# Performance work log

Hardware: AMD Instinct MI355X
Metric: run time of the kernel (lower is better)

The kernel has to match this reference:

```python
import jax, jax.numpy as jnp
import numpy as np
import math

B, S, HID = 2, 2048, 1024
NH = 16
HD = HID // NH


def setup_inputs() -> dict:
    key = jax.random.key(0)
    ks = jax.random.split(key, 5)
    std = 1.0 / math.sqrt(HID)
    return {
        "x": jax.random.normal(ks[0], (B, S, HID), dtype=jnp.float32),
        "wq": jax.random.normal(ks[1], (HID, HID), dtype=jnp.float32) * std,
        "wk": jax.random.normal(ks[2], (HID, HID), dtype=jnp.float32) * std,
        "wv": jax.random.normal(ks[3], (HID, HID), dtype=jnp.float32) * std,
        "wo": jax.random.normal(ks[4], (HID, HID), dtype=jnp.float32) * std,
    }


def reference(x, wq, wk, wv, wo):
    # x: [B, S, HID]; weights stored as nn.Linear weight [out, in] -> y = x @ W.T
    b, s, _ = x.shape
    scale = 1.0 / math.sqrt(HD)

    def heads(t):  # [B, S, HID] -> [B, NH, S, HD]
        return t.reshape(b, s, NH, HD).transpose(0, 2, 1, 3)

    q = heads(x @ wq.T)
    k = heads(x @ wk.T)
    v = heads(x @ wv.T)

    # single ring step (cp_size=1): streaming-LSE causal attention
    scores = jnp.einsum("bhqd,bhkd->bhqk", q, k) * scale  # [B, NH, S, S]
    q_idx = jnp.arange(s)[:, None]
    k_idx = jnp.arange(s)[None, :]
    causal_mask = k_idx > q_idx  # [S, S]
    scores = jnp.where(causal_mask, -jnp.inf, scores)

    local_max = jnp.max(scores, axis=-1, keepdims=True)
    exp_scores = jnp.exp(scores - local_max)
    local_sum = jnp.sum(exp_scores, axis=-1, keepdims=True)
    attn_num = jnp.einsum("bhqk,bhkd->bhqd", exp_scores, v)
    attn_out = attn_num / (local_sum + 1e-8)  # [B, NH, S, HD]

    attn_out = attn_out.transpose(0, 2, 1, 3).reshape(b, s, HID)
    return attn_out @ wo.T
```

## Files before the change

kernel.cpp:

```cpp
#include <hip/hip_runtime.h>
#include <hip/hip_bf16.h>

#define S_LEN 2048
#define NHEAD 16
#define HDIM 64
#define HID 1024
#define BATCH 2
#define TSTR 136

typedef __attribute__((ext_vector_type(8))) short s16x8;
typedef __attribute__((ext_vector_type(4))) short s16x4;
typedef __attribute__((ext_vector_type(4))) float f32x4;

__device__ __forceinline__ short f2bf(float f) {
    union { __hip_bfloat16 b; short s; } u;
    u.b = __float2bfloat16(f);
    return u.s;
}
__device__ __forceinline__ float fexp2(float x) {
    return __builtin_amdgcn_exp2f(x);
}
__device__ __forceinline__ f32x4 mfma16(s16x8 a, s16x8 b, f32x4 c) {
    return __builtin_amdgcn_mfma_f32_16x16x32_bf16(a, b, c, 0, 0, 0);
}
__device__ __forceinline__ void gload16(const short* g, short* l) {
    __builtin_amdgcn_global_load_lds(
        (const __attribute__((address_space(1))) void*)g,
        (__attribute__((address_space(3))) void*)l, 16, 0, 0);
}
__device__ __forceinline__ unsigned bfpack(float a, float b) {
    unsigned ua = __builtin_bit_cast(unsigned, a) + 0x8000u;
    unsigned ub = __builtin_bit_cast(unsigned, b) + 0x8000u;
    return (ub & 0xFFFF0000u) | (ua >> 16);
}

__global__ __launch_bounds__(256) void convert_kernel(
    const float* __restrict__ x,  const float* __restrict__ wq,
    const float* __restrict__ wk, const float* __restrict__ wv,
    const float* __restrict__ wo,
    short* __restrict__ xb, short* __restrict__ wcat, short* __restrict__ wob)
{
    const int F4X = 1048576, F4W = 262144;
    const int total = F4X + 4 * F4W;
    for (int i = blockIdx.x * blockDim.x + threadIdx.x; i < total;
         i += gridDim.x * blockDim.x) {
        const float4* s; short* d; int off;
        if (i < F4X)              { s = (const float4*)x;  d = xb;             off = i; }
        else if (i < F4X + F4W)   { s = (const float4*)wq; d = wcat;           off = i - F4X; }
        else if (i < F4X + 2*F4W) { s = (const float4*)wk; d = wcat + 1048576; off = i - (F4X + F4W); }
        else if (i < F4X + 3*F4W) { s = (const float4*)wv; d = wcat + 2097152; off = i - (F4X + 2*F4W); }
        else                      { s = (const float4*)wo; d = wob;            off = i - (F4X + 3*F4W); }
        float4 v = s[off];
        s16x4 o4 = { f2bf(v.x), f2bf(v.y), f2bf(v.z), f2bf(v.w) };
        *(s16x4*)(d + (size_t)off * 4) = o4;
    }
}

__global__ __launch_bounds__(256) void qkv_gemm2(
    const short* __restrict__ xb, const short* __restrict__ wcat,
    short* __restrict__ q_ws, short* __restrict__ k_ws, short* __restrict__ vt_ws)
{
    __shared__ union SM {
        struct { short A[128][64]; short B[128][64]; } s;
        short T[128][TSTR];
    } sm;
    const int t = threadIdx.x;
    const int lane = t & 63, w = t >> 6;
    const int g = lane >> 4, r15 = lane & 15;
    const int wm = w >> 1, wn = w & 1;
    const int bid = blockIdx.x;
    const int cx = bid & 7, ii = bid >> 3;
    const int mt = cx * 4 + (ii & 3), nt = ii >> 2;
    const int m0 = mt * 128, n0 = nt * 128;
    const int sel = n0 >> 10;
    const int nr0 = n0 & 1023;
    const short* Ag = (sel == 2) ? (wcat + (size_t)(2048 + nr0) * 1024)
                                 : (xb   + (size_t)m0 * 1024);
    const short* Bg = (sel == 2) ? (xb   + (size_t)m0 * 1024)
                                 : (wcat + (size_t)(sel * 1024 + nr0) * 1024);
    const int lrow = lane >> 3;
    const int scol = ((lane & 7) ^ lrow) * 8;
    const int rsw = r15 & 7;
    const float osc = (sel == 0) ? 0.125f : ((sel == 1) ? 1.44269504f : 1.0f);

    f32x4 acc[4][4] = {};

    for (int k0 = 0; k0 < 1024; k0 += 64) {
        __syncthreads();
        #pragma unroll
        for (int ch = 0; ch < 4; ++ch) {
            const int row = w * 32 + ch * 8;
            gload16(Ag + (size_t)(row + lrow) * 1024 + k0 + scol, &sm.s.A[row][0]);
            gload16(Bg + (size_t)(row + lrow) * 1024 + k0 + scol, &sm.s.B[row][0]);
        }
        __syncthreads();
        #pragma unroll
        for (int kk = 0; kk < 2; ++kk) {
            s16x8 af[4], bfr[4];
            #pragma unroll
            for (int mi = 0; mi < 4; ++mi)
                af[mi] = *(const s16x8*)&sm.s.A[wm * 64 + mi * 16 + r15][((kk * 4 + g) ^ rsw) * 8];
            #pragma unroll
            for (int ni = 0; ni < 4; ++ni)
                bfr[ni] = *(const s16x8*)&sm.s.B[wn * 64 + ni * 16 + r15][((kk * 4 + g) ^ rsw) * 8];
            #pragma unroll
            for (int mi = 0; mi < 4; ++mi)
                #pragma unroll
                for (int ni = 0; ni < 4; ++ni)
                    acc[mi][ni] = mfma16(af[mi], bfr[ni], acc[mi][ni]);
        }
    }

    __syncthreads();
    #pragma unroll
    for (int mi = 0; mi < 4; ++mi)
    #pragma unroll
    for (int ni = 0; ni < 4; ++ni)
        #pragma unroll
        for (int reg = 0; reg < 4; ++reg)
            sm.T[wm * 64 + mi * 16 + g * 4 + reg][wn * 64 + ni * 16 + r15]
                = f2bf(acc[mi][ni][reg] * osc);
    __syncthreads();

    const int b = m0 >> 11;
    const int ms = m0 & 2047;
    #pragma unroll
    for (int it = 0; it < 8; ++it) {
        int u = w + it * 4;
        int half = u & 1;
        int rg = u >> 1;
        int r = rg * 8 + lrow;
        int colc = half * 64 + (lane & 7) * 8;
        s16x8 v = *(const s16x8*)&sm.T[r][colc];
        if (sel == 2) {
            int n = nr0 + r;
            int h = n >> 6, d = n & 63;
            *(s16x8*)(vt_ws + ((size_t)(b * NHEAD + h) * HDIM + d) * S_LEN + ms + colc) = v;
        } else {
            int s = ms + r;
            int n = nr0 + colc;
            int h = n >> 6, d = n & 63;
            short* dst = (sel == 0) ? q_ws : k_ws;
            *(s16x8*)(dst + ((size_t)(b * NHEAD + h) * S_LEN + s) * HDIM + d) = v;
        }
    }
}

__global__ __launch_bounds__(256) void attn_kernel11(
    const short* __restrict__ q_ws, const short* __restrict__ k_ws,
    const short* __restrict__ vt_ws, short* __restrict__ attn_ws)
{
    __shared__ short Ks[2][64][64];
    __shared__ short Vts[2][64][64];
    const int t = threadIdx.x;
    const int lane = t & 63, w = t >> 6;
    const int g = lane >> 4, r15 = lane & 15;
    const int bid = blockIdx.x;
    const int lb = (bid & 7) * 32 + (bid >> 3);
    const int pi = lb & 7;
    const int bh = lb >> 3;
    const size_t base = (size_t)bh * S_LEN * HDIM;
    const int swr = (r15 & 7) << 3;
    const int b = bh >> 4, h = bh & 15;

    const int r0 = t >> 3, c0 = (t & 7) * 8;
    const int cx0 = c0 ^ ((r0 & 7) << 3);

    union P8 { unsigned u[4]; s16x8 v; };
    union V8 { s16x4 h[2]; s16x8 v; };

    for (int phase = 0; phase < 2; ++phase) {
        const int qt = phase ? (15 - pi) : pi;
        const int q0 = qt * 128;
        const int ntk = 2 * qt + 2;
        const int dgt = 2 * qt + (w >> 1);
        const int qrel = (w & 1) * 32 + r15;

        s16x8 qf[2][2];
        #pragma unroll
        for (int m = 0; m < 2; ++m)
            #pragma unroll
            for (int c = 0; c < 2; ++c)
                qf[m][c] = *(const s16x8*)(q_ws + base +
                    (size_t)(q0 + w * 32 + m * 16 + r15) * HDIM + c * 32 + g * 8);
        f32x4 o[2][4] = {};
        float lr[2] = { 0.f, 0.f };

        #pragma unroll
        for (int j = 0; j < 2; ++j) {
            int r = r0 + j * 32;
            *(s16x8*)&Ks[0][r][cx0]  = *(const s16x8*)(k_ws  + base + (size_t)r * HDIM + c0);
            *(s16x8*)&Vts[0][r][cx0] = *(const s16x8*)(vt_ws + base + (size_t)r * S_LEN + c0);
        }
        __syncthreads();

        const short* kp = k_ws  + base + (size_t)(64 + r0) * HDIM + c0;
        const short* vp = vt_ws + base + (size_t)r0 * S_LEN + 64 + c0;

        for (int kt = 0; kt < ntk; ++kt) {
            const int cur = kt & 1;
            const bool pre = (kt + 1 < ntk);
            s16x8 ka[2], va[2];
            if (pre) {
                ka[0] = *(const s16x8*)kp;
                ka[1] = *(const s16x8*)(kp + (size_t)32 * HDIM);
                va[0] = *(const s16x8*)vp;
                va[1] = *(const s16x8*)(vp + (size_t)32 * S_LEN);
                kp += (size_t)64 * HDIM; vp += 64;
            }

            if (kt <= dgt) {
                const bool dg = (kt == dgt);

                s16x8 kfa[4][2];
                #pragma unroll
                for (int f = 0; f < 4; ++f)
                    #pragma unroll
                    for (int c = 0; c < 2; ++c)
                        kfa[f][c] = *(const s16x8*)&Ks[cur][f * 16 + r15][(c * 32 + g * 8) ^ swr];
                V8 vfr[4][2];
                #pragma unroll
                for (int f2 = 0; f2 < 4; ++f2)
                    #pragma unroll
                    for (int kc = 0; kc < 2; ++kc) {
                        vfr[f2][kc].h[0] = *(const s16x4*)&Vts[cur][f2 * 16 + r15][(kc * 32 + g * 4) ^ swr];
                        vfr[f2][kc].h[1] = *(const s16x4*)&Vts[cur][f2 * 16 + r15][(kc * 32 + 16 + g * 4) ^ swr];
                    }

                #pragma unroll
                for (int m = 0; m < 2; ++m) {
                    f32x4 z[4];
                    __builtin_amdgcn_s_setprio(1);
                    #pragma unroll
                    for (int f = 0; f < 4; ++f) {
                        f32x4 zz = { 0.f, 0.f, 0.f, 0.f };
                        zz = mfma16(kfa[f][0], qf[m][0], zz);
                        zz = mfma16(kfa[f][1], qf[m][1], zz);
                        z[f] = zz;
                    }
                    __builtin_amdgcn_s_setprio(0);

                    if (dg) {
                        const int qr = qrel + m * 16;
                        #pragma unroll
                        for (int f = 0; f < 4; ++f)
                            #pragma unroll
                            for (int reg = 0; reg < 4; ++reg)
                                if (f * 16 + g * 4 + reg > qr) z[f][reg] = -3e30f;
                    }

                    P8 p8[2];
                    #pragma unroll
                    for (int f = 0; f < 4; ++f) {
                        float e0 = fexp2(z[f][0]);
                        float e1 = fexp2(z[f][1]);
                        float e2 = fexp2(z[f][2]);
                        float e3 = fexp2(z[f][3]);
                        lr[m] += (e0 + e1) + (e2 + e3);
                        p8[f >> 1].u[(f & 1) * 2]     = bfpack(e0, e1);
                        p8[f >> 1].u[(f & 1) * 2 + 1] = bfpack(e2, e3);
                    }

                    __builtin_amdgcn_s_setprio(1);
                    #pragma unroll
                    for (int f2 = 0; f2 < 4; ++f2) {
                        o[m][f2] = mfma16(vfr[f2][0].v, p8[0].v, o[m][f2]);
                        o[m][f2] = mfma16(vfr[f2][1].v, p8[1].v, o[m][f2]);
                    }
                    __builtin_amdgcn_s_setprio(0);
                }
            }

            if (pre) {
                #pragma unroll
                for (int j = 0; j < 2; ++j) {
                    int r = r0 + j * 32;
                    *(s16x8*)&Ks[cur ^ 1][r][cx0]  = ka[j];
                    *(s16x8*)&Vts[cur ^ 1][r][cx0] = va[j];
                }
            }
            __syncthreads();
        }

        #pragma unroll
        for (int m = 0; m < 2; ++m) {
            float l = lr[m];
            l += __shfl_xor(l, 16);
            l += __shfl_xor(l, 32);
            float inv = 1.f / (l + 1e-8f);
            const int qg = q0 + w * 32 + m * 16 + r15;
            size_t obase = ((size_t)b * S_LEN + qg) * HID + h * HDIM + g * 4;
            #pragma unroll
            for (int f2 = 0; f2 < 4; ++f2) {
                s16x4 ov = { f2bf(o[m][f2][0] * inv), f2bf(o[m][f2][1] * inv),
                             f2bf(o[m][f2][2] * inv), f2bf(o[m][f2][3] * inv) };
                *(s16x4*)(attn_ws + obase + f2 * 16) = ov;
            }
        }
        __syncthreads();
    }
}

__global__ __launch_bounds__(256) void wo_gemm2(
    const short* __restrict__ attn, const short* __restrict__ wob,
    float* __restrict__ out)
{
    __shared__ short As[128][64];
    __shared__ short Bs[128][64];
    const int t = threadIdx.x;
    const int lane = t & 63, w = t >> 6;
    const int g = lane >> 4, r15 = lane & 15;
    const int wm = w >> 1, wn = w & 1;
    const int bid = blockIdx.x;
    const int cx = bid & 7, ii = bid >> 3;
    const int mt = cx * 4 + (ii & 3), nt = ii >> 2;
    const int m0 = mt * 128, n0 = nt * 128;
    const int lrow = lane >> 3;
    const int scol = ((lane & 7) ^ lrow) * 8;
    const int rsw = r15 & 7;

    f32x4 acc[4][4] = {};

    for (int k0 = 0; k0 < 1024; k0 += 64) {
        __syncthreads();
        #pragma unroll
        for (int ch = 0; ch < 4; ++ch) {
            const int row = w * 32 + ch * 8;
            gload16(attn + (size_t)(m0 + row + lrow) * 1024 + k0 + scol, &As[row][0]);
            gload16(wob  + (size_t)(n0 + row + lrow) * 1024 + k0 + scol, &Bs[row][0]);
        }
        __syncthreads();
        #pragma unroll
        for (int kk = 0; kk < 2; ++kk) {
            s16x8 af[4], bfr[4];
            #pragma unroll
            for (int mi = 0; mi < 4; ++mi)
                af[mi] = *(const s16x8*)&As[wm * 64 + mi * 16 + r15][((kk * 4 + g) ^ rsw) * 8];
            #pragma unroll
            for (int ni = 0; ni < 4; ++ni)
                bfr[ni] = *(const s16x8*)&Bs[wn * 64 + ni * 16 + r15][((kk * 4 + g) ^ rsw) * 8];
            #pragma unroll
            for (int mi = 0; mi < 4; ++mi)
                #pragma unroll
                for (int ni = 0; ni < 4; ++ni)
                    acc[mi][ni] = mfma16(af[mi], bfr[ni], acc[mi][ni]);
        }
    }

    #pragma unroll
    for (int mi = 0; mi < 4; ++mi)
    #pragma unroll
    for (int ni = 0; ni < 4; ++ni) {
        #pragma unroll
        for (int reg = 0; reg < 4; ++reg) {
            int m = m0 + wm * 64 + mi * 16 + g * 4 + reg;
            int n = n0 + wn * 64 + ni * 16 + r15;
            out[(size_t)m * 1024 + n] = acc[mi][ni][reg];
        }
    }
}

extern "C" void kernel_launch(void* const* d_in, const int* in_sizes, int n_in,
                              void* d_out, int out_size, void* d_ws, size_t ws_size,
                              hipStream_t stream) {
    const float* x  = (const float*)d_in[0];
    const float* wq = (const float*)d_in[1];
    const float* wk = (const float*)d_in[2];
    const float* wv = (const float*)d_in[3];
    const float* wo = (const float*)d_in[4];
    float* out = (float*)d_out;

    const size_t ELEMS = (size_t)BATCH * S_LEN * HID;
    short* q_ws    = (short*)d_ws;
    short* k_ws    = q_ws + ELEMS;
    short* vt_ws   = k_ws + ELEMS;
    short* xb      = vt_ws + ELEMS;
    short* attn_ws = xb;
    short* wcat    = xb + ELEMS;
    short* wob     = wcat + 3145728;

    convert_kernel<<<dim3(2048), dim3(256), 0, stream>>>(x, wq, wk, wv, wo, xb, wcat, wob);
    qkv_gemm2<<<dim3(768), dim3(256), 0, stream>>>(xb, wcat, q_ws, k_ws, vt_ws);
    attn_kernel11<<<dim3(256), dim3(256), 0, stream>>>(q_ws, k_ws, vt_ws, attn_ws);
    wo_gemm2<<<dim3(256), dim3(256), 0, stream>>>(attn_ws, wob, out);
}
```

Measured before the change: 117.5 us.

## Software-pipeline attention by deferring PV MFMAs one key tile

The attention loop now issues the P·V matrix multiplies for the previous key tile at the start of the next iteration, before the QK^T and exp work for the current tile. The loop is unrolled by two, with ping-pong V fragment register buffers, and probabilities are kept in registers for both row groups. A tail step finishes the last deferred PV for the warps whose last active tile is the final one. The aim is to overlap the exp/pack vector work with matrix-core work and hide LDS-read latency, at the cost of more live registers and possibly lower occupancy.

```diff
diff --git a/kernel.cpp b/kernel.cpp
--- a/kernel.cpp
+++ b/kernel.cpp
@@ -33,6 +33,9 @@
     unsigned ub = __builtin_bit_cast(unsigned, b) + 0x8000u;
     return (ub & 0xFFFF0000u) | (ua >> 16);
 }
+
+union P8 { unsigned u[4]; s16x8 v; };
+union V8 { s16x4 h[2]; s16x8 v; };
 
 __global__ __launch_bounds__(256) void convert_kernel(
     const float* __restrict__ x,  const float* __restrict__ wq,
@@ -146,7 +149,7 @@
     }
 }
 
-__global__ __launch_bounds__(256) void attn_kernel11(
+__global__ __launch_bounds__(256) void attn_kernel12(
     const short* __restrict__ q_ws, const short* __restrict__ k_ws,
     const short* __restrict__ vt_ws, short* __restrict__ attn_ws)
 {
@@ -166,9 +169,6 @@
     const int r0 = t >> 3, c0 = (t & 7) * 8;
     const int cx0 = c0 ^ ((r0 & 7) << 3);
 
-    union P8 { unsigned u[4]; s16x8 v; };
-    union V8 { s16x4 h[2]; s16x8 v; };
-
     for (int phase = 0; phase < 2; ++phase) {
         const int qt = phase ? (15 - pi) : pi;
         const int q0 = qt * 128;
@@ -185,6 +185,8 @@
                     (size_t)(q0 + w * 32 + m * 16 + r15) * HDIM + c * 32 + g * 8);
         f32x4 o[2][4] = {};
         float lr[2] = { 0.f, 0.f };
+        P8 pm8[2][2];
+        V8 vfA[4][2], vfB[4][2];
 
         #pragma unroll
         for (int j = 0; j < 2; ++j) {
@@ -197,8 +199,7 @@
         const short* kp = k_ws  + base + (size_t)(64 + r0) * HDIM + c0;
         const short* vp = vt_ws + base + (size_t)r0 * S_LEN + 64 + c0;
 
-        for (int kt = 0; kt < ntk; ++kt) {
-            const int cur = kt & 1;
+        auto STEP = [&](int kt, int cur, V8 (&VC)[4][2], V8 (&VP)[4][2]) {
             const bool pre = (kt + 1 < ntk);
             s16x8 ka[2], va[2];
             if (pre) {
@@ -208,25 +209,38 @@
                 va[1] = *(const s16x8*)(vp + (size_t)32 * S_LEN);
                 kp += (size_t)64 * HDIM; vp += 64;
             }
-
-            if (kt <= dgt) {
-                const bool dg = (kt == dgt);
-
-                s16x8 kfa[4][2];
+            const bool active = (kt <= dgt);
+
+            s16x8 kfa[4][2];
+            if (active) {
                 #pragma unroll
                 for (int f = 0; f < 4; ++f)
                     #pragma unroll
                     for (int c = 0; c < 2; ++c)
                         kfa[f][c] = *(const s16x8*)&Ks[cur][f * 16 + r15][(c * 32 + g * 8) ^ swr];
-                V8 vfr[4][2];
                 #pragma unroll
                 for (int f2 = 0; f2 < 4; ++f2)
                     #pragma unroll
                     for (int kc = 0; kc < 2; ++kc) {
-                        vfr[f2][kc].h[0] = *(const s16x4*)&Vts[cur][f2 * 16 + r15][(kc * 32 + g * 4) ^ swr];
-                        vfr[f2][kc].h[1] = *(const s16x4*)&Vts[cur][f2 * 16 + r15][(kc * 32 + 16 + g * 4) ^ swr];
+                        VC[f2][kc].h[0] = *(const s16x4*)&Vts[cur][f2 * 16 + r15][(kc * 32 + g * 4) ^ swr];
+                        VC[f2][kc].h[1] = *(const s16x4*)&Vts[cur][f2 * 16 + r15][(kc * 32 + 16 + g * 4) ^ swr];
                     }
-
+            }
+
+            if (kt >= 1 && kt <= dgt + 1) {
+                __builtin_amdgcn_s_setprio(1);
+                #pragma unroll
+                for (int m = 0; m < 2; ++m)
+                    #pragma unroll
+                    for (int f2 = 0; f2 < 4; ++f2) {
+                        o[m][f2] = mfma16(VP[f2][0].v, pm8[m][0].v, o[m][f2]);
+                        o[m][f2] = mfma16(VP[f2][1].v, pm8[m][1].v, o[m][f2]);
+                    }
+                __builtin_amdgcn_s_setprio(0);
+            }
+
+            if (active) {
+                const bool dg = (kt == dgt);
                 #pragma unroll
                 for (int m = 0; m < 2; ++m) {
                     f32x4 z[4];
@@ -239,7 +253,6 @@
                         z[f] = zz;
                     }
                     __builtin_amdgcn_s_setprio(0);
-
                     if (dg) {
                         const int qr = qrel + m * 16;
                         #pragma unroll
@@ -248,8 +261,6 @@
                             for (int reg = 0; reg < 4; ++reg)
                                 if (f * 16 + g * 4 + reg > qr) z[f][reg] = -3e30f;
                     }
-
-                    P8 p8[2];
                     #pragma unroll
                     for (int f = 0; f < 4; ++f) {
                         float e0 = fexp2(z[f][0]);
@@ -257,17 +268,9 @@
                         float e2 = fexp2(z[f][2]);
                         float e3 = fexp2(z[f][3]);
                         lr[m] += (e0 + e1) + (e2 + e3);
-                        p8[f >> 1].u[(f & 1) * 2]     = bfpack(e0, e1);
-                        p8[f >> 1].u[(f & 1) * 2 + 1] = bfpack(e2, e3);
+                        pm8[m][f >> 1].u[(f & 1) * 2]     = bfpack(e0, e1);
+                        pm8[m][f >> 1].u[(f & 1) * 2 + 1] = bfpack(e2, e3);
                     }
-
-                    __builtin_amdgcn_s_setprio(1);
-                    #pragma unroll
-                    for (int f2 = 0; f2 < 4; ++f2) {
-                        o[m][f2] = mfma16(vfr[f2][0].v, p8[0].v, o[m][f2]);
-                        o[m][f2] = mfma16(vfr[f2][1].v, p8[1].v, o[m][f2]);
-                    }
-                    __builtin_amdgcn_s_setprio(0);
                 }
             }
 
@@ -280,6 +283,21 @@
                 }
             }
             __syncthreads();
+        };
+
+        for (int kt2 = 0; kt2 < ntk; kt2 += 2) {
+            STEP(kt2,     0, vfA, vfB);
+            STEP(kt2 + 1, 1, vfB, vfA);
+        }
+
+        if ((w >> 1) == 1) {
+            #pragma unroll
+            for (int m = 0; m < 2; ++m)
+                #pragma unroll
+                for (int f2 = 0; f2 < 4; ++f2) {
+                    o[m][f2] = mfma16(vfB[f2][0].v, pm8[m][0].v, o[m][f2]);
+                    o[m][f2] = mfma16(vfB[f2][1].v, pm8[m][1].v, o[m][f2]);
+                }
         }
 
         #pragma unroll
@@ -381,6 +399,6 @@
 
     convert_kernel<<<dim3(2048), dim3(256), 0, stream>>>(x, wq, wk, wv, wo, xb, wcat, wob);
     qkv_gemm2<<<dim3(768), dim3(256), 0, stream>>>(xb, wcat, q_ws, k_ws, vt_ws);
-    attn_kernel11<<<dim3(256), dim3(256), 0, stream>>>(q_ws, k_ws, vt_ws, attn_ws);
+    attn_kernel12<<<dim3(256), dim3(256), 0, stream>>>(q_ws, k_ws, vt_ws, attn_ws);
     wo_gemm2<<<dim3(256), dim3(256), 0, stream>>>(attn_ws, wob, out);
 }
```

Result: no change. 119.5 us (+1.7%).

## Enlarge QKV GEMM tile to 128x256 and halve the grid

Applied to the files above, without the earlier changes.

The QKV projection GEMM moves from 128x128 tiles over 768 blocks to 128x256 tiles over 384 blocks. Each wave now owns a 128x64 output slice with 8x4 accumulators, and the epilogue writes back in two halves through the shared transpose buffer. The goal is more arithmetic per byte loaded from global memory and fewer blocks. In exchange it needs more registers and shared memory, which may lower occupancy, and 384 blocks may fill the CUs less evenly.

```diff
diff --git a/kernel.cpp b/kernel.cpp
--- a/kernel.cpp
+++ b/kernel.cpp
@@ -33,6 +33,9 @@
     unsigned ub = __builtin_bit_cast(unsigned, b) + 0x8000u;
     return (ub & 0xFFFF0000u) | (ua >> 16);
 }
+
+union P8 { unsigned u[4]; s16x8 v; };
+union V8 { s16x4 h[2]; s16x8 v; };
 
 __global__ __launch_bounds__(256) void convert_kernel(
     const float* __restrict__ x,  const float* __restrict__ wq,
@@ -56,34 +59,42 @@
     }
 }
 
-__global__ __launch_bounds__(256) void qkv_gemm2(
+__global__ __launch_bounds__(256) void qkv_gemm3(
     const short* __restrict__ xb, const short* __restrict__ wcat,
     short* __restrict__ q_ws, short* __restrict__ k_ws, short* __restrict__ vt_ws)
 {
     __shared__ union SM {
-        struct { short A[128][64]; short B[128][64]; } s;
+        struct { short A[128][64]; short B[256][64]; } s;
         short T[128][TSTR];
     } sm;
     const int t = threadIdx.x;
     const int lane = t & 63, w = t >> 6;
     const int g = lane >> 4, r15 = lane & 15;
-    const int wm = w >> 1, wn = w & 1;
     const int bid = blockIdx.x;
     const int cx = bid & 7, ii = bid >> 3;
-    const int mt = cx * 4 + (ii & 3), nt = ii >> 2;
-    const int m0 = mt * 128, n0 = nt * 128;
-    const int sel = n0 >> 10;
-    const int nr0 = n0 & 1023;
-    const short* Ag = (sel == 2) ? (wcat + (size_t)(2048 + nr0) * 1024)
-                                 : (xb   + (size_t)m0 * 1024);
-    const short* Bg = (sel == 2) ? (xb   + (size_t)m0 * 1024)
-                                 : (wcat + (size_t)(sel * 1024 + nr0) * 1024);
+    const int mt = cx * 4 + (ii & 3);
+    const int nt = ii >> 2;
+    const int sel = nt >> 2;
     const int lrow = lane >> 3;
     const int scol = ((lane & 7) ^ lrow) * 8;
     const int rsw = r15 & 7;
+
+    const short* Ag; const short* Bg;
+    int dtile = 0, stile = 0, m0 = 0, nr0 = 0;
+    if (sel == 2) {
+        int idx = (nt - 8) * 32 + mt;
+        dtile = idx >> 4;
+        stile = idx & 15;
+        Ag = wcat + (size_t)(2048 + dtile * 128) * 1024;
+        Bg = xb   + (size_t)stile * 256 * 1024;
+    } else {
+        m0 = mt * 128; nr0 = (nt & 3) * 256;
+        Ag = xb   + (size_t)m0 * 1024;
+        Bg = wcat + (size_t)(sel * 1024 + nr0) * 1024;
+    }
     const float osc = (sel == 0) ? 0.125f : ((sel == 1) ? 1.44269504f : 1.0f);
 
-    f32x4 acc[4][4] = {};
+    f32x4 acc[8][4] = {};
 
     for (int k0 = 0; k0 < 1024; k0 += 64) {
         __syncthreads();
@@ -91,58 +102,68 @@
         for (int ch = 0; ch < 4; ++ch) {
             const int row = w * 32 + ch * 8;
             gload16(Ag + (size_t)(row + lrow) * 1024 + k0 + scol, &sm.s.A[row][0]);
+        }
+        #pragma unroll
+        for (int ch = 0; ch < 8; ++ch) {
+            const int row = w * 64 + ch * 8;
             gload16(Bg + (size_t)(row + lrow) * 1024 + k0 + scol, &sm.s.B[row][0]);
         }
         __syncthreads();
         #pragma unroll
         for (int kk = 0; kk < 2; ++kk) {
-            s16x8 af[4], bfr[4];
-            #pragma unroll
-            for (int mi = 0; mi < 4; ++mi)
-                af[mi] = *(const s16x8*)&sm.s.A[wm * 64 + mi * 16 + r15][((kk * 4 + g) ^ rsw) * 8];
+            s16x8 bfr[4];
             #pragma unroll
             for (int ni = 0; ni < 4; ++ni)
-                bfr[ni] = *(const s16x8*)&sm.s.B[wn * 64 + ni * 16 + r15][((kk * 4 + g) ^ rsw) * 8];
-            #pragma unroll
-            for (int mi = 0; mi < 4; ++mi)
+                bfr[ni] = *(const s16x8*)&sm.s.B[w * 64 + ni * 16 + r15][((kk * 4 + g) ^ rsw) * 8];
+            #pragma unroll
+            for (int mi = 0; mi < 8; ++mi) {
+                s16x8 af = *(const s16x8*)&sm.s.A[mi * 16 + r15][((kk * 4 + g) ^ rsw) * 8];
                 #pragma unroll
                 for (int ni = 0; ni < 4; ++ni)
-                    acc[mi][ni] = mfma16(af[mi], bfr[ni], acc[mi][ni]);
+                    acc[mi][ni] = mfma16(af, bfr[ni], acc[mi][ni]);
+            }
         }
     }
 
     __syncthreads();
-    #pragma unroll
-    for (int mi = 0; mi < 4; ++mi)
-    #pragma unroll
-    for (int ni = 0; ni < 4; ++ni)
-        #pragma unroll
-        for (int reg = 0; reg < 4; ++reg)
-            sm.T[wm * 64 + mi * 16 + g * 4 + reg][wn * 64 + ni * 16 + r15]
-                = f2bf(acc[mi][ni][reg] * osc);
-    __syncthreads();
-
-    const int b = m0 >> 11;
+    const int b0 = m0 >> 11;
     const int ms = m0 & 2047;
     #pragma unroll
-    for (int it = 0; it < 8; ++it) {
-        int u = w + it * 4;
-        int half = u & 1;
-        int rg = u >> 1;
-        int r = rg * 8 + lrow;
-        int colc = half * 64 + (lane & 7) * 8;
-        s16x8 v = *(const s16x8*)&sm.T[r][colc];
-        if (sel == 2) {
-            int n = nr0 + r;
-            int h = n >> 6, d = n & 63;
-            *(s16x8*)(vt_ws + ((size_t)(b * NHEAD + h) * HDIM + d) * S_LEN + ms + colc) = v;
-        } else {
-            int s = ms + r;
-            int n = nr0 + colc;
-            int h = n >> 6, d = n & 63;
-            short* dst = (sel == 0) ? q_ws : k_ws;
-            *(s16x8*)(dst + ((size_t)(b * NHEAD + h) * S_LEN + s) * HDIM + d) = v;
-        }
+    for (int ph = 0; ph < 2; ++ph) {
+        if ((w >> 1) == ph) {
+            #pragma unroll
+            for (int mi = 0; mi < 8; ++mi)
+                #pragma unroll
+                for (int ni = 0; ni < 4; ++ni)
+                    #pragma unroll
+                    for (int reg = 0; reg < 4; ++reg)
+                        sm.T[mi * 16 + g * 4 + reg][(w & 1) * 64 + ni * 16 + r15]
+                            = f2bf(acc[mi][ni][reg] * osc);
+        }
+        __syncthreads();
+        #pragma unroll
+        for (int it = 0; it < 8; ++it) {
+            int u = w + it * 4;
+            int half = u & 1;
+            int rg = u >> 1;
+            int r = rg * 8 + lrow;
+            int colc = half * 64 + (lane & 7) * 8;
+            s16x8 v = *(const s16x8*)&sm.T[r][colc];
+            if (sel == 2) {
+                int d = dtile * 128 + r;
+                int h2 = d >> 6, dl = d & 63;
+                int sg = stile * 256 + ph * 128 + colc;
+                int b = sg >> 11, sl = sg & 2047;
+                *(s16x8*)(vt_ws + ((size_t)(b * NHEAD + h2) * HDIM + dl) * S_LEN + sl) = v;
+            } else {
+                int s = ms + r;
+                int n = nr0 + ph * 128 + colc;
+                int h2 = n >> 6, d = n & 63;
+                short* dst = (sel == 0) ? q_ws : k_ws;
+                *(s16x8*)(dst + ((size_t)(b0 * NHEAD + h2) * S_LEN + s) * HDIM + d) = v;
+            }
+        }
+        __syncthreads();
     }
 }
 
@@ -165,9 +186,6 @@
 
     const int r0 = t >> 3, c0 = (t & 7) * 8;
     const int cx0 = c0 ^ ((r0 & 7) << 3);
-
-    union P8 { unsigned u[4]; s16x8 v; };
-    union V8 { s16x4 h[2]; s16x8 v; };
 
     for (int phase = 0; phase < 2; ++phase) {
         const int qt = phase ? (15 - pi) : pi;
@@ -380,7 +398,7 @@
     short* wob     = wcat + 3145728;
 
     convert_kernel<<<dim3(2048), dim3(256), 0, stream>>>(x, wq, wk, wv, wo, xb, wcat, wob);
-    qkv_gemm2<<<dim3(768), dim3(256), 0, stream>>>(xb, wcat, q_ws, k_ws, vt_ws);
+    qkv_gemm3<<<dim3(384), dim3(256), 0, stream>>>(xb, wcat, q_ws, k_ws, vt_ws);
     attn_kernel11<<<dim3(256), dim3(256), 0, stream>>>(q_ws, k_ws, vt_ws, attn_ws);
     wo_gemm2<<<dim3(256), dim3(256), 0, stream>>>(attn_ws, wob, out);
 }
```

New measurement: 138.7 us. 1.18x slower.
